# Kernel tuning notes

Measured on AMD Instinct MI355X. Metric: run time of the kernel, lower is better.

The kernel has to match this reference:

```python
import jax, jax.numpy as jnp
import numpy as np

DIM = 1024
HEADS = 8
NUM_KEYS = 256
TOPK = 32
D_HEAD = DIM // HEADS
BATCH = 2
SEQ = 2048


def setup_inputs() -> dict:
    key = jax.random.key(0)
    ks = jax.random.split(key, 5)
    x = jax.random.normal(ks[0], (BATCH, SEQ, DIM), jnp.float32)
    # nn.Linear(dim, 2*dim, bias=False): weight (2*dim, dim)
    Wq = jax.random.normal(ks[1], (2 * DIM, DIM), jnp.float32) * (DIM ** -0.5)
    # nn.Parameter(torch.randn(heads, num_keys, 2, d_head))
    keys = jax.random.normal(ks[2], (HEADS, NUM_KEYS, 2, D_HEAD), jnp.float32)
    # nn.Parameter(torch.randn(heads, num_keys**2, d_head))
    values = jax.random.normal(ks[3], (HEADS, NUM_KEYS ** 2, D_HEAD), jnp.float32)
    # nn.Linear(dim, dim): weight (dim, dim), bias (dim,)
    Wo = jax.random.normal(ks[4], (DIM, DIM), jnp.float32) * (DIM ** -0.5)
    bo = jnp.zeros((DIM,), jnp.float32)
    return {"x": x, "Wq": Wq, "keys": keys, "values": values, "Wo": Wo, "bo": bo}


def reference(x, Wq, keys, values, Wo, bo):
    b, t, e = x.shape
    h, dh, k, nk = HEADS, D_HEAD, TOPK, NUM_KEYS
    # to_queries + chunk(2, dim=-1) + stack -> (2, b, t, h, d_head)
    q = x @ Wq.T                                    # (b, t, 2*dim)
    q = q.reshape(b, t, 2, e).transpose(2, 0, 1, 3)  # (2, b, t, dim), matches chunk+stack
    q = q.reshape(2, b, t, h, dh)
    # dual sub-key scores: (b, h, t, 2, num_keys)
    dots = jnp.einsum('pbthd,hnpd->bhtpn', q, keys)
    # top-k over num_keys per sub-key
    scores, indices = jax.lax.top_k(dots, k)         # (b, h, t, 2, k)
    # faithful to source: chunk(2, dim=2) splits the TIME axis
    th = t // 2
    s0, s1 = scores[:, :, :th], scores[:, :, th:]
    i0, i1 = indices[:, :, :th], indices[:, :, th:]
    # Cartesian combination: (b, h, t//2, 2, k, k) -> (b, h, t, k*k)
    all_scores = (s0[..., :, None] + s1[..., None, :]).reshape(b, h, t, k * k)
    all_indices = (i0[..., :, None] * nk + i1[..., None, :]).reshape(b, h, t, k * k)
    # final top-k over the k^2 candidates
    final_scores, final_idx = jax.lax.top_k(all_scores, k)   # (b, h, t, k)
    value_indices = jnp.take_along_axis(all_indices, final_idx, axis=-1)  # (b, h, t, k)
    attn = jax.nn.softmax(final_scores, axis=-1)
    # gather values per head: values (h, nk^2, dh), idx (b, h, t, k) -> (b, h, t, k, dh)
    sel = jax.vmap(lambda v, idx: v[idx], in_axes=(0, 1), out_axes=1)(values, value_indices)
    out = jnp.einsum('bhtk,bhtkd->bhtd', attn, sel)  # weighted sum over top-k
    out = out.transpose(0, 2, 1, 3).reshape(b, t, e)
    return out @ Wo.T + bo
```

## Files before the change

kernel.cpp:

```cpp
#include <hip/hip_runtime.h>

typedef unsigned int u32;
typedef unsigned long long u64;
typedef _Float16 f16;
typedef __attribute__((ext_vector_type(4))) _Float16 f16x4;
typedef __attribute__((ext_vector_type(8))) _Float16 f16x8;
typedef __attribute__((ext_vector_type(4))) float f32x4;
typedef const __attribute__((address_space(1))) void* gp_t;
typedef __attribute__((address_space(3))) void* lp_t;

#define TSEQ 2048

__device__ __forceinline__ u32 f2sort(float f) {
  u32 u = __float_as_uint(f);
  return u ^ ((u32)((int)u >> 31) | 0x80000000u);
}
__device__ __forceinline__ float sort2f(u32 u) {
  u ^= (u & 0x80000000u) ? 0x80000000u : 0xFFFFFFFFu;
  return __uint_as_float(u);
}

__device__ __forceinline__ void glds16(const f16* g, f16* l) {
  __builtin_amdgcn_global_load_lds((gp_t)g, (lp_t)l, 16, 0, 0);
}

__global__ __launch_bounds__(256) void cvt_all(
    const float* __restrict__ x, const float* __restrict__ wq,
    const float* __restrict__ wo, const float* __restrict__ ky,
    f16* __restrict__ xd, f16* __restrict__ wqd, f16* __restrict__ wod,
    f16* __restrict__ kyd) {
  int g = blockIdx.x * 256 + threadIdx.x;
  const float* s;
  f16* d;
  int off;
  if (g < 1048576)      { s = x;  d = xd;  off = g; }
  else if (g < 1572864) { s = wq; d = wqd; off = g - 1048576; }
  else if (g < 1835008) { s = wo; d = wod; off = g - 1572864; }
  else                  { s = ky; d = kyd; off = g - 1835008; }
  float4 v = ((const float4*)s)[off];
  f16x4 o;
  o[0] = (f16)v.x; o[1] = (f16)v.y; o[2] = (f16)v.z; o[3] = (f16)v.w;
  ((f16x4*)d)[off] = o;
}

__global__ __launch_bounds__(256) void gemm_f16(
    const f16* __restrict__ A, int lda, const f16* __restrict__ B, int ldb,
    const float* __restrict__ bias, void* __restrict__ Cv, int ldc, int K,
    int c_f16) {
  __shared__ f16 As[128 * 32];
  __shared__ f16 Bs[128 * 32];
  const int tid = threadIdx.x;
  const int lane = tid & 63, wave = tid >> 6;
  const int m0 = blockIdx.y << 7, n0 = blockIdx.x << 7;
  const int c0 = wave * 128 + lane, c1 = c0 + 64;
  const int r0 = c0 >> 2, s0 = c0 & 3;
  const int r1 = c1 >> 2, s1 = c1 & 3;
  const f16* Ab = A + (size_t)m0 * lda;
  const f16* Bb = B + (size_t)n0 * ldb;
  const int fm = lane & 15, fq = lane >> 4, fk = fq << 3;
  const int wm = (wave >> 1) << 6, wn = (wave & 1) << 6;
  f32x4 acc[4][4] = {};
  for (int k0 = 0; k0 < K; k0 += 32) {
    __syncthreads();
    glds16(Ab + (size_t)r0 * lda + k0 + s0 * 8, As + (size_t)c0 * 8 - lane * 8);
    glds16(Ab + (size_t)r1 * lda + k0 + s1 * 8, As + (size_t)c1 * 8 - lane * 8);
    glds16(Bb + (size_t)r0 * ldb + k0 + s0 * 8, Bs + (size_t)c0 * 8 - lane * 8);
    glds16(Bb + (size_t)r1 * ldb + k0 + s1 * 8, Bs + (size_t)c1 * 8 - lane * 8);
    __syncthreads();
    f16x8 af[4], bf[4];
#pragma unroll
    for (int mi = 0; mi < 4; mi++)
      af[mi] = *(const f16x8*)&As[(wm + mi * 16 + fm) * 32 + fk];
#pragma unroll
    for (int nj = 0; nj < 4; nj++)
      bf[nj] = *(const f16x8*)&Bs[(wn + nj * 16 + fm) * 32 + fk];
#pragma unroll
    for (int mi = 0; mi < 4; mi++)
#pragma unroll
      for (int nj = 0; nj < 4; nj++)
        acc[mi][nj] = __builtin_amdgcn_mfma_f32_16x16x32_f16(
            af[mi], bf[nj], acc[mi][nj], 0, 0, 0);
  }
  if (c_f16) {
    f16* C = (f16*)Cv;
#pragma unroll
    for (int mi = 0; mi < 4; mi++)
#pragma unroll
      for (int r = 0; r < 4; r++) {
        int row = m0 + wm + mi * 16 + fq * 4 + r;
        f16* cp = C + (size_t)row * ldc + n0 + wn + fm;
#pragma unroll
        for (int nj = 0; nj < 4; nj++) cp[nj * 16] = (f16)acc[mi][nj][r];
      }
  } else {
    float* C = (float*)Cv;
    float bb[4];
#pragma unroll
    for (int nj = 0; nj < 4; nj++)
      bb[nj] = bias ? bias[n0 + wn + nj * 16 + fm] : 0.f;
#pragma unroll
    for (int mi = 0; mi < 4; mi++)
#pragma unroll
      for (int r = 0; r < 4; r++) {
        int row = m0 + wm + mi * 16 + fq * 4 + r;
        float* cp = C + (size_t)row * ldc + n0 + wn + fm;
#pragma unroll
        for (int nj = 0; nj < 4; nj++) cp[nj * 16] = acc[mi][nj][r] + bb[nj];
      }
  }
}

__global__ __launch_bounds__(256) void dots_topk1(
    const f16* __restrict__ Q,
    const f16* __restrict__ keysf,
    float* __restrict__ s1s, int* __restrict__ s1i) {
  __shared__ f16 As[64 * 32];
  __shared__ f16 Bs[256 * 32];
  const int tid = threadIdx.x;
  const int lane = tid & 63, wave = tid >> 6;
  const int z = blockIdx.y;
  const int h = z >> 1, p = z & 1;
  const int m0 = blockIdx.x << 6;
  const f16* Aq = Q + (size_t)m0 * 2048 + p * 1024 + h * 128;
  const f16* Bk = keysf + ((size_t)h * 512 + p) * 128;
  const int cA = wave * 64 + lane;
  const int rA = cA >> 2, sA = cA & 3;
  const int fm = lane & 15, fq = lane >> 4, fk = fq << 3;
  f32x4 acc[16] = {};
  for (int k0 = 0; k0 < 128; k0 += 32) {
    __syncthreads();
    glds16(Aq + (size_t)rA * 2048 + k0 + sA * 8, As + (size_t)cA * 8 - lane * 8);
#pragma unroll
    for (int c = 0; c < 4; c++) {
      int cB = (wave * 4 + c) * 64 + lane;
      int rB = cB >> 2, sB = cB & 3;
      glds16(Bk + (size_t)rB * 256 + k0 + sB * 8,
             Bs + (size_t)cB * 8 - lane * 8);
    }
    __syncthreads();
    f16x8 af = *(const f16x8*)&As[(wave * 16 + fm) * 32 + fk];
#pragma unroll
    for (int j = 0; j < 16; j++) {
      f16x8 bf = *(const f16x8*)&Bs[(j * 16 + fm) * 32 + fk];
      acc[j] = __builtin_amdgcn_mfma_f32_16x16x32_f16(af, bf, acc[j], 0, 0, 0);
    }
  }
  const int grp = lane & 48;
  for (int r = 0; r < 4; r++) {
    u32 key[16];
#pragma unroll
    for (int j = 0; j < 16; j++)
      key[j] = (f2sort(acc[j][r]) & ~0xFFu) | (u32)j;
    float myw0 = 0.f, myw1 = 0.f;
    int myi0 = 0, myi1 = 0;
    for (int it = 0; it < 32; it++) {
      u32 lm = key[0];
#pragma unroll
      for (int j = 1; j < 16; j++) lm = key[j] > lm ? key[j] : lm;
      u32 gm = lm;
#pragma unroll
      for (int d = 1; d < 16; d <<= 1) {
        u32 o = (u32)__shfl_xor((int)gm, d);
        gm = o > gm ? o : gm;
      }
      u64 mask = __ballot(lm == gm);
      int owner = __ffsll((u64)((mask >> grp) & 0xFFFFull)) - 1;
      int swin = (int)(gm & 0xFFu);
      int idx = swin * 16 + owner;
      float score = sort2f(gm & ~0xFFu);
      bool isown = (fm == owner);
#pragma unroll
      for (int j = 0; j < 16; j++)
        key[j] = (isown && j == swin) ? 0u : key[j];
      if (fm == (it & 15)) {
        if (it < 16) { myw0 = score; myi0 = idx; }
        else         { myw1 = score; myi1 = idx; }
      }
    }
    int m = m0 + wave * 16 + (fq << 2) + r;
    int b = m >> 11, t = m & 2047;
    size_t orow = ((((size_t)(b * 8 + h)) * TSEQ + t) * 2 + p) * 32;
    s1s[orow + fm] = myw0;
    s1s[orow + fm + 16] = myw1;
    s1i[orow + fm] = myi0;
    s1i[orow + fm + 16] = myi1;
  }
}

__global__ __launch_bounds__(256) void topk2_gather(
    const float* __restrict__ s1s, const int* __restrict__ s1i,
    const float* __restrict__ values, f16* __restrict__ headout) {
  __shared__ unsigned short cand[128];
  __shared__ float s0sh[16][32];
  __shared__ float s1sh[16][32];
  __shared__ int i0sh[16][32];
  __shared__ int i1sh[16][32];
  const int tid = threadIdx.x;
  if (tid < 128) {
    int c = tid;
    unsigned short enc = 0xFFFF;
    if (c < 119) {
      int rem = c, i = 0;
      for (i = 0; i < 32; i++) {
        int cnt = 32 / (i + 1);
        if (rem < cnt) break;
        rem -= cnt;
      }
      enc = (unsigned short)((i << 5) | rem);
    }
    cand[tid] = enc;
  }
  const int rloc = tid >> 4;
  const int l = tid & 15;
  const int row = blockIdx.x * 16 + rloc;
  const int b = row >> 14;
  const int h = (row >> 11) & 7;
  const int t = row & 2047;
  const int tt = t >> 1, p = t & 1;
  size_t rbase = (size_t)(b * 8 + h) * TSEQ;
  size_t base0 = ((rbase + tt) * 2 + p) * 32;
  size_t base1 = ((rbase + tt + 1024) * 2 + p) * 32;
  s0sh[rloc][l] = s1s[base0 + l];
  s0sh[rloc][l + 16] = s1s[base0 + l + 16];
  s1sh[rloc][l] = s1s[base1 + l];
  s1sh[rloc][l + 16] = s1s[base1 + l + 16];
  i0sh[rloc][l] = s1i[base0 + l];
  i0sh[rloc][l + 16] = s1i[base0 + l + 16];
  i1sh[rloc][l] = s1i[base1 + l];
  i1sh[rloc][l + 16] = s1i[base1 + l + 16];
  __syncthreads();
  u32 key[8];
#pragma unroll
  for (int s = 0; s < 8; s++) {
    int c = l + 16 * s;
    unsigned short e = cand[c];
    u32 kk = 0u;
    if (e != 0xFFFF) {
      float v = s0sh[rloc][e >> 5] + s1sh[rloc][e & 31];
      kk = (f2sort(v) & ~0xFFu) | (u32)s;
    }
    key[s] = kk;
  }
  const int grp = tid & 48;
  float myw0 = 0.f, myw1 = 0.f;
  int myv0 = 0, myv1 = 0;
  for (int it = 0; it < 32; it++) {
    u32 lm = key[0];
#pragma unroll
    for (int s = 1; s < 8; s++) lm = key[s] > lm ? key[s] : lm;
    u32 gm = lm;
#pragma unroll
    for (int d = 1; d < 16; d <<= 1) {
      u32 o = (u32)__shfl_xor((int)gm, d);
      gm = o > gm ? o : gm;
    }
    u64 mask = __ballot(lm == gm);
    int owner = __ffsll((u64)((mask >> grp) & 0xFFFFull)) - 1;
    int swin = (int)(gm & 0xFFu);
    unsigned short e = cand[owner + 16 * swin];
    int wi = e >> 5, wj = e & 31;
    float score = sort2f(gm & ~0xFFu);
    int vidx = i0sh[rloc][wi] * 256 + i1sh[rloc][wj];
    bool isown = (l == owner);
#pragma unroll
    for (int s = 0; s < 8; s++)
      key[s] = (isown && s == swin) ? 0u : key[s];
    if (l == (it & 15)) {
      if (it < 16) { myw0 = score; myv0 = vidx; }
      else         { myw1 = score; myv1 = vidx; }
    }
  }
  float m0 = __shfl(myw0, grp);
  float e0 = __expf(myw0 - m0);
  float e1 = __expf(myw1 - m0);
  float ssum = e0 + e1;
#pragma unroll
  for (int d = 1; d < 16; d <<= 1) ssum += __shfl_xor(ssum, d);
  float inv = 1.0f / ssum;
  float a0 = e0 * inv, a1 = e1 * inv;
  const float* vb = values + (((size_t)h) << 16) * 128 + l * 8;
  float4 acc0 = make_float4(0.f, 0.f, 0.f, 0.f);
  float4 acc1 = make_float4(0.f, 0.f, 0.f, 0.f);
#pragma unroll 8
  for (int k = 0; k < 32; k++) {
    int src = grp + (k & 15);
    int vi = __shfl((k < 16) ? myv0 : myv1, src);
    float wk = __shfl((k < 16) ? a0 : a1, src);
    const float* vp = vb + (size_t)vi * 128;
    float4 x0 = *(const float4*)(vp);
    float4 x1 = *(const float4*)(vp + 4);
    acc0.x += wk * x0.x; acc0.y += wk * x0.y;
    acc0.z += wk * x0.z; acc0.w += wk * x0.w;
    acc1.x += wk * x1.x; acc1.y += wk * x1.y;
    acc1.z += wk * x1.z; acc1.w += wk * x1.w;
  }
  f16x8 o;
  o[0] = (f16)acc0.x; o[1] = (f16)acc0.y; o[2] = (f16)acc0.z; o[3] = (f16)acc0.w;
  o[4] = (f16)acc1.x; o[5] = (f16)acc1.y; o[6] = (f16)acc1.z; o[7] = (f16)acc1.w;
  f16* op = headout + (size_t)(b * TSEQ + t) * 1024 + h * 128 + l * 8;
  *(f16x8*)op = o;
}

extern "C" void kernel_launch(void* const* d_in, const int* in_sizes, int n_in,
                              void* d_out, int out_size, void* d_ws,
                              size_t ws_size, hipStream_t stream) {
  const float* x    = (const float*)d_in[0];
  const float* Wq   = (const float*)d_in[1];
  const float* keys = (const float*)d_in[2];
  const float* vals = (const float*)d_in[3];
  const float* Wo   = (const float*)d_in[4];
  const float* bo   = (const float*)d_in[5];
  float* out = (float*)d_out;
  char* ws = (char*)d_ws;
  f16*   xf  = (f16*)(ws);
  f16*   wqf = (f16*)(ws + (size_t)(8u << 20));
  f16*   wof = (f16*)(ws + (size_t)(12u << 20));
  f16*   kyf = (f16*)(ws + (size_t)(14u << 20));
  f16*   Qf  = (f16*)(ws + (size_t)(16u << 20));
  float* s1s = (float*)(ws + (size_t)(32u << 20));
  int*   s1i = (int*)(ws + (size_t)(40u << 20));
  f16*   hof = (f16*)(ws + (size_t)(48u << 20));

  cvt_all<<<dim3(7680), 256, 0, stream>>>(x, Wq, Wo, keys, xf, wqf, wof, kyf);
  gemm_f16<<<dim3(16, 32), 256, 0, stream>>>(xf, 1024, wqf, 1024, nullptr, Qf,
                                             2048, 1024, 1);
  dots_topk1<<<dim3(64, 16), 256, 0, stream>>>(Qf, kyf, s1s, s1i);
  topk2_gather<<<dim3(32768 / 16), 256, 0, stream>>>(s1s, s1i, vals, hof);
  gemm_f16<<<dim3(8, 32), 256, 0, stream>>>(hof, 1024, wof, 1024, bo, out,
                                            1024, 1024, 0);
}
```

Measured before the change: 570.3 us.

## Gather f16 values, use DPP reductions with packed indices in top-k loops

Values are converted to f16 in the conversion kernel on every call, so the top-k gather reads half as many bytes per selected row. The cost is a full read and write of the large values table each call. Both top-k selection loops now pack the candidate index into the low bits of the sort key. This lets a DPP/swizzle max reduction replace the shuffle, ballot and owner-finding logic. The gather stages indices and softmax weights in LDS instead of shuffling them per step, and the dots kernel's grid axes are swapped.

New measurement: 566.7 us. Within noise of the previous version (-0.6%).

```diff
diff --git a/kernel.cpp b/kernel.cpp
--- a/kernel.cpp
+++ b/kernel.cpp
@@ -24,16 +24,46 @@
   __builtin_amdgcn_global_load_lds((gp_t)g, (lp_t)l, 16, 0, 0);
 }
 
+__device__ __forceinline__ u32 dppmax16(u32 v) {
+  u32 t;
+  t = (u32)__builtin_amdgcn_update_dpp(0, (int)v, 0x111, 0xF, 0xF, true);
+  v = v > t ? v : t;
+  t = (u32)__builtin_amdgcn_update_dpp(0, (int)v, 0x112, 0xF, 0xF, true);
+  v = v > t ? v : t;
+  t = (u32)__builtin_amdgcn_update_dpp(0, (int)v, 0x114, 0xF, 0xF, true);
+  v = v > t ? v : t;
+  t = (u32)__builtin_amdgcn_update_dpp(0, (int)v, 0x118, 0xF, 0xF, true);
+  v = v > t ? v : t;
+  return (u32)__builtin_amdgcn_ds_swizzle((int)v, 0x1F0);
+}
+__device__ __forceinline__ float dppsum16(float v) {
+  float t;
+  t = __int_as_float(
+      __builtin_amdgcn_update_dpp(0, __float_as_int(v), 0x111, 0xF, 0xF, true));
+  v += t;
+  t = __int_as_float(
+      __builtin_amdgcn_update_dpp(0, __float_as_int(v), 0x112, 0xF, 0xF, true));
+  v += t;
+  t = __int_as_float(
+      __builtin_amdgcn_update_dpp(0, __float_as_int(v), 0x114, 0xF, 0xF, true));
+  v += t;
+  t = __int_as_float(
+      __builtin_amdgcn_update_dpp(0, __float_as_int(v), 0x118, 0xF, 0xF, true));
+  v += t;
+  return __int_as_float(__builtin_amdgcn_ds_swizzle(__float_as_int(v), 0x1F0));
+}
+
 __global__ __launch_bounds__(256) void cvt_all(
     const float* __restrict__ x, const float* __restrict__ wq,
     const float* __restrict__ wo, const float* __restrict__ ky,
-    f16* __restrict__ xd, f16* __restrict__ wqd, f16* __restrict__ wod,
-    f16* __restrict__ kyd) {
+    const float* __restrict__ vl, f16* __restrict__ xd, f16* __restrict__ wqd,
+    f16* __restrict__ wod, f16* __restrict__ kyd, f16* __restrict__ vld) {
   int g = blockIdx.x * 256 + threadIdx.x;
   const float* s;
   f16* d;
   int off;
-  if (g < 1048576)      { s = x;  d = xd;  off = g; }
+  if (g >= 1966080)     { s = vl; d = vld; off = g - 1966080; }
+  else if (g < 1048576) { s = x;  d = xd;  off = g; }
   else if (g < 1572864) { s = wq; d = wqd; off = g - 1048576; }
   else if (g < 1835008) { s = wo; d = wod; off = g - 1572864; }
   else                  { s = ky; d = kyd; off = g - 1835008; }
@@ -118,9 +148,9 @@
   __shared__ f16 Bs[256 * 32];
   const int tid = threadIdx.x;
   const int lane = tid & 63, wave = tid >> 6;
-  const int z = blockIdx.y;
+  const int z = blockIdx.x;
   const int h = z >> 1, p = z & 1;
-  const int m0 = blockIdx.x << 6;
+  const int m0 = blockIdx.y << 6;
   const f16* Aq = Q + (size_t)m0 * 2048 + p * 1024 + h * 128;
   const f16* Bk = keysf + ((size_t)h * 512 + p) * 128;
   const int cA = wave * 64 + lane;
@@ -145,56 +175,43 @@
       acc[j] = __builtin_amdgcn_mfma_f32_16x16x32_f16(af, bf, acc[j], 0, 0, 0);
     }
   }
-  const int grp = lane & 48;
   for (int r = 0; r < 4; r++) {
     u32 key[16];
 #pragma unroll
     for (int j = 0; j < 16; j++)
-      key[j] = (f2sort(acc[j][r]) & ~0xFFu) | (u32)j;
-    float myw0 = 0.f, myw1 = 0.f;
-    int myi0 = 0, myi1 = 0;
+      key[j] = (f2sort(acc[j][r]) & ~0xFFu) | (u32)((j << 4) | fm);
+    u32 g0 = 0, g1 = 0;
     for (int it = 0; it < 32; it++) {
       u32 lm = key[0];
 #pragma unroll
       for (int j = 1; j < 16; j++) lm = key[j] > lm ? key[j] : lm;
-      u32 gm = lm;
-#pragma unroll
-      for (int d = 1; d < 16; d <<= 1) {
-        u32 o = (u32)__shfl_xor((int)gm, d);
-        gm = o > gm ? o : gm;
-      }
-      u64 mask = __ballot(lm == gm);
-      int owner = __ffsll((u64)((mask >> grp) & 0xFFFFull)) - 1;
-      int swin = (int)(gm & 0xFFu);
-      int idx = swin * 16 + owner;
-      float score = sort2f(gm & ~0xFFu);
-      bool isown = (fm == owner);
-#pragma unroll
-      for (int j = 0; j < 16; j++)
-        key[j] = (isown && j == swin) ? 0u : key[j];
-      if (fm == (it & 15)) {
-        if (it < 16) { myw0 = score; myi0 = idx; }
-        else         { myw1 = score; myi1 = idx; }
-      }
+      u32 gm = dppmax16(lm);
+#pragma unroll
+      for (int j = 0; j < 16; j++) key[j] = (key[j] == gm) ? 0u : key[j];
+      bool sel = (fm == (it & 15));
+      if (it < 16) g0 = sel ? gm : g0;
+      else         g1 = sel ? gm : g1;
     }
     int m = m0 + wave * 16 + (fq << 2) + r;
     int b = m >> 11, t = m & 2047;
     size_t orow = ((((size_t)(b * 8 + h)) * TSEQ + t) * 2 + p) * 32;
-    s1s[orow + fm] = myw0;
-    s1s[orow + fm + 16] = myw1;
-    s1i[orow + fm] = myi0;
-    s1i[orow + fm + 16] = myi1;
+    s1s[orow + fm] = sort2f(g0 & ~0xFFu);
+    s1s[orow + fm + 16] = sort2f(g1 & ~0xFFu);
+    s1i[orow + fm] = (int)(g0 & 0xFFu);
+    s1i[orow + fm + 16] = (int)(g1 & 0xFFu);
   }
 }
 
 __global__ __launch_bounds__(256) void topk2_gather(
     const float* __restrict__ s1s, const int* __restrict__ s1i,
-    const float* __restrict__ values, f16* __restrict__ headout) {
+    const f16* __restrict__ valf, f16* __restrict__ headout) {
   __shared__ unsigned short cand[128];
   __shared__ float s0sh[16][32];
   __shared__ float s1sh[16][32];
   __shared__ int i0sh[16][32];
   __shared__ int i1sh[16][32];
+  __shared__ int vtab[16][32];
+  __shared__ float wtab[16][32];
   const int tid = threadIdx.x;
   if (tid < 128) {
     int c = tid;
@@ -237,66 +254,50 @@
     u32 kk = 0u;
     if (e != 0xFFFF) {
       float v = s0sh[rloc][e >> 5] + s1sh[rloc][e & 31];
-      kk = (f2sort(v) & ~0xFFu) | (u32)s;
+      kk = (f2sort(v) & ~0xFFu) | (u32)c;
     }
     key[s] = kk;
   }
-  const int grp = tid & 48;
-  float myw0 = 0.f, myw1 = 0.f;
-  int myv0 = 0, myv1 = 0;
+  u32 g0 = 0, g1 = 0;
   for (int it = 0; it < 32; it++) {
     u32 lm = key[0];
 #pragma unroll
     for (int s = 1; s < 8; s++) lm = key[s] > lm ? key[s] : lm;
-    u32 gm = lm;
-#pragma unroll
-    for (int d = 1; d < 16; d <<= 1) {
-      u32 o = (u32)__shfl_xor((int)gm, d);
-      gm = o > gm ? o : gm;
-    }
-    u64 mask = __ballot(lm == gm);
-    int owner = __ffsll((u64)((mask >> grp) & 0xFFFFull)) - 1;
-    int swin = (int)(gm & 0xFFu);
-    unsigned short e = cand[owner + 16 * swin];
-    int wi = e >> 5, wj = e & 31;
-    float score = sort2f(gm & ~0xFFu);
-    int vidx = i0sh[rloc][wi] * 256 + i1sh[rloc][wj];
-    bool isown = (l == owner);
-#pragma unroll
-    for (int s = 0; s < 8; s++)
-      key[s] = (isown && s == swin) ? 0u : key[s];
-    if (l == (it & 15)) {
-      if (it < 16) { myw0 = score; myv0 = vidx; }
-      else         { myw1 = score; myv1 = vidx; }
-    }
-  }
-  float m0 = __shfl(myw0, grp);
-  float e0 = __expf(myw0 - m0);
-  float e1 = __expf(myw1 - m0);
-  float ssum = e0 + e1;
-#pragma unroll
-  for (int d = 1; d < 16; d <<= 1) ssum += __shfl_xor(ssum, d);
-  float inv = 1.0f / ssum;
-  float a0 = e0 * inv, a1 = e1 * inv;
-  const float* vb = values + (((size_t)h) << 16) * 128 + l * 8;
-  float4 acc0 = make_float4(0.f, 0.f, 0.f, 0.f);
-  float4 acc1 = make_float4(0.f, 0.f, 0.f, 0.f);
+    u32 gm = dppmax16(lm);
+#pragma unroll
+    for (int s = 0; s < 8; s++) key[s] = (key[s] == gm) ? 0u : key[s];
+    bool sel = (l == (it & 15));
+    if (it < 16) g0 = sel ? gm : g0;
+    else         g1 = sel ? gm : g1;
+  }
+  float sc0 = sort2f(g0 & ~0xFFu);
+  float sc1 = sort2f(g1 & ~0xFFu);
+  unsigned short e0c = cand[g0 & 0xFFu];
+  unsigned short e1c = cand[g1 & 0xFFu];
+  int vidx0 = i0sh[rloc][e0c >> 5] * 256 + i1sh[rloc][e0c & 31];
+  int vidx1 = i0sh[rloc][e1c >> 5] * 256 + i1sh[rloc][e1c & 31];
+  float mx = __int_as_float(
+      __builtin_amdgcn_ds_swizzle(__float_as_int(sc0), 0x010));
+  float e0 = __expf(sc0 - mx);
+  float e1 = __expf(sc1 - mx);
+  float inv = 1.0f / dppsum16(e0 + e1);
+  vtab[rloc][l] = vidx0;
+  vtab[rloc][l + 16] = vidx1;
+  wtab[rloc][l] = e0 * inv;
+  wtab[rloc][l + 16] = e1 * inv;
+  const f16* vb = valf + (((size_t)h) << 16) * 128 + l * 8;
+  float accf[8] = {};
 #pragma unroll 8
   for (int k = 0; k < 32; k++) {
-    int src = grp + (k & 15);
-    int vi = __shfl((k < 16) ? myv0 : myv1, src);
-    float wk = __shfl((k < 16) ? a0 : a1, src);
-    const float* vp = vb + (size_t)vi * 128;
-    float4 x0 = *(const float4*)(vp);
-    float4 x1 = *(const float4*)(vp + 4);
-    acc0.x += wk * x0.x; acc0.y += wk * x0.y;
-    acc0.z += wk * x0.z; acc0.w += wk * x0.w;
-    acc1.x += wk * x1.x; acc1.y += wk * x1.y;
-    acc1.z += wk * x1.z; acc1.w += wk * x1.w;
+    int vi = vtab[rloc][k];
+    float wk = wtab[rloc][k];
+    f16x8 vv = *(const f16x8*)(vb + (size_t)vi * 128);
+#pragma unroll
+    for (int j = 0; j < 8; j++) accf[j] += wk * (float)vv[j];
   }
   f16x8 o;
-  o[0] = (f16)acc0.x; o[1] = (f16)acc0.y; o[2] = (f16)acc0.z; o[3] = (f16)acc0.w;
-  o[4] = (f16)acc1.x; o[5] = (f16)acc1.y; o[6] = (f16)acc1.z; o[7] = (f16)acc1.w;
+#pragma unroll
+  for (int j = 0; j < 8; j++) o[j] = (f16)accf[j];
   f16* op = headout + (size_t)(b * TSEQ + t) * 1024 + h * 128 + l * 8;
   *(f16x8*)op = o;
 }
@@ -312,20 +313,22 @@
   const float* bo   = (const float*)d_in[5];
   float* out = (float*)d_out;
   char* ws = (char*)d_ws;
-  f16*   xf  = (f16*)(ws);
-  f16*   wqf = (f16*)(ws + (size_t)(8u << 20));
-  f16*   wof = (f16*)(ws + (size_t)(12u << 20));
-  f16*   kyf = (f16*)(ws + (size_t)(14u << 20));
-  f16*   Qf  = (f16*)(ws + (size_t)(16u << 20));
-  float* s1s = (float*)(ws + (size_t)(32u << 20));
-  int*   s1i = (int*)(ws + (size_t)(40u << 20));
-  f16*   hof = (f16*)(ws + (size_t)(48u << 20));
-
-  cvt_all<<<dim3(7680), 256, 0, stream>>>(x, Wq, Wo, keys, xf, wqf, wof, kyf);
+  f16*   xf   = (f16*)(ws);
+  f16*   wqf  = (f16*)(ws + (size_t)(8u << 20));
+  f16*   wof  = (f16*)(ws + (size_t)(12u << 20));
+  f16*   kyf  = (f16*)(ws + (size_t)(14u << 20));
+  f16*   Qf   = (f16*)(ws + (size_t)(16u << 20));
+  float* s1s  = (float*)(ws + (size_t)(32u << 20));
+  int*   s1i  = (int*)(ws + (size_t)(40u << 20));
+  f16*   hof  = (f16*)(ws + (size_t)(48u << 20));
+  f16*   valf = (f16*)(ws + (size_t)(64u << 20));
+
+  cvt_all<<<dim3(73216), 256, 0, stream>>>(x, Wq, Wo, keys, vals, xf, wqf, wof,
+                                           kyf, valf);
   gemm_f16<<<dim3(16, 32), 256, 0, stream>>>(xf, 1024, wqf, 1024, nullptr, Qf,
                                              2048, 1024, 1);
-  dots_topk1<<<dim3(64, 16), 256, 0, stream>>>(Qf, kyf, s1s, s1i);
-  topk2_gather<<<dim3(32768 / 16), 256, 0, stream>>>(s1s, s1i, vals, hof);
+  dots_topk1<<<dim3(16, 64), 256, 0, stream>>>(Qf, kyf, s1s, s1i);
+  topk2_gather<<<dim3(32768 / 16), 256, 0, stream>>>(s1s, s1i, valf, hof);
   gemm_f16<<<dim3(8, 32), 256, 0, stream>>>(hof, 1024, wof, 1024, bo, out,
                                             1024, 1024, 0);
 }
```
